# Kernel tuning notes

Hardware: AMD Instinct MI355X
Metric: run time of the kernel (lower is better)

## Reference

```python
import jax, jax.numpy as jnp
import numpy as np

MAX_NODES = 1024
FEAT = 64
HID = 32
B, S = 32, 4096


def setup_inputs() -> dict:
    key = jax.random.key(0)
    ks = jax.random.split(key, 9)
    flow_features = jax.random.normal(ks[0], (B, S, FEAT), dtype=jnp.float32)
    src_ips = jax.random.randint(ks[1], (B, S), 0, MAX_NODES, dtype=jnp.int32)
    dst_ips = jax.random.randint(ks[2], (B, S), 0, MAX_NODES, dtype=jnp.int32)
    flow_volumes = jax.random.uniform(ks[3], (B, S), dtype=jnp.float32)
    # learned parameters
    node_emb = jax.random.normal(ks[4], (MAX_NODES, FEAT), dtype=jnp.float32)
    W1 = jax.random.normal(ks[5], (2 * FEAT, HID), dtype=jnp.float32) * (1.0 / np.sqrt(2 * FEAT))
    b1 = jnp.zeros((HID,), dtype=jnp.float32)
    W2 = jax.random.normal(ks[6], (HID, 1), dtype=jnp.float32) * (1.0 / np.sqrt(HID))
    b2 = jnp.zeros((1,), dtype=jnp.float32)
    return {"flow_features": flow_features, "src_ips": src_ips, "dst_ips": dst_ips,
            "flow_volumes": flow_volumes, "node_emb": node_emb,
            "W1": W1, "b1": b1, "W2": W2, "b2": b2}


def reference(flow_features, src_ips, dst_ips, flow_volumes, node_emb, W1, b1, W2, b2):
    b_, s_, f_ = flow_features.shape
    n_ = node_emb.shape[0]
    bidx = jnp.arange(b_)[:, None]  # (B,1) broadcast over seq

    # ---- scatter-add flow features into destination nodes ----
    node_features = jnp.zeros((b_, n_, f_), dtype=flow_features.dtype)
    node_features = node_features.at[bidx, dst_ips].add(flow_features)
    # F.normalize(p=2, dim=-1): x / max(||x||, eps)
    norm = jnp.linalg.norm(node_features, axis=-1, keepdims=True)
    node_features = node_features / jnp.maximum(norm, 1e-12)

    # ---- gather embeddings, edge MLP, scatter weights into adjacency ----
    src_e = node_emb[src_ips]  # (B,S,F)
    dst_e = node_emb[dst_ips]  # (B,S,F)
    h = jax.nn.relu(jnp.concatenate([src_e, dst_e], axis=-1) @ W1 + b1)  # (B,S,32)
    edge_w = jax.nn.sigmoid((h @ W2 + b2)[..., 0])  # (B,S)
    vol_w = jax.nn.sigmoid(flow_volumes / 1000.0)
    w = edge_w * vol_w  # (B,S)

    adjacency = jnp.zeros((b_, n_, n_), dtype=flow_features.dtype)
    # semantics up to scatter ordering of colliding edges)
    adjacency = adjacency.at[bidx, src_ips, dst_ips].set(w)
    adjacency = adjacency.at[bidx, dst_ips, src_ips].set(w)
    return node_features, adjacency
```

## Files before the change

### kernel.cpp

```cpp
#include <hip/hip_runtime.h>
#include <cstdint>
#include <cstddef>

#define BB 32
#define SS 4096
#define FEAT_ 64
#define HID_ 32
#define NN 1024
#define RPB 8

typedef int v4i __attribute__((ext_vector_type(4)));

__global__ void node_feat_kernel(const float* __restrict__ flow,
                                 const int* __restrict__ dst,
                                 float* __restrict__ nf) {
    int row0 = blockIdx.x << 4;
    int b = row0 >> 10;
    __shared__ int sdst[SS];

    const int4* g = (const int4*)(dst + (size_t)b * SS);
    int4* sd4 = (int4*)sdst;
    for (int i = threadIdx.x; i < SS / 4; i += 256) sd4[i] = g[i];
    __syncthreads();

    int wave = threadIdx.x >> 6;
    int lane = threadIdx.x & 63;
    int r0 = row0 + (wave << 2);
    int node0 = r0 & (NN - 1);
    const float* fb = flow + ((size_t)b * SS << 6);

    float acc[4] = {0.f, 0.f, 0.f, 0.f};
    for (int s0 = 0; s0 < SS; s0 += 64) {
        int d = sdst[s0 + lane];
        #pragma unroll
        for (int j = 0; j < 4; ++j) {
            unsigned long long m = __ballot(d == node0 + j);
            while (m) {
                int bit = __ffsll((long long)m) - 1;
                m &= m - 1;
                acc[j] += fb[((s0 + bit) << 6) + lane];
            }
        }
    }

    #pragma unroll
    for (int j = 0; j < 4; ++j) {
        float ss = acc[j] * acc[j];
        #pragma unroll
        for (int off = 32; off > 0; off >>= 1) ss += __shfl_xor(ss, off, 64);
        float v = acc[j] / fmaxf(sqrtf(ss), 1e-12f);
        __builtin_nontemporal_store(v, &nf[((size_t)(r0 + j) << 6) + lane]);
    }
}

__global__ void mlp_kernel(const int* __restrict__ src,
                           const int* __restrict__ dst,
                           const float* __restrict__ vol,
                           const float* __restrict__ emb,
                           const float* __restrict__ W1,
                           const float* __restrict__ b1,
                           const float* __restrict__ W2,
                           const float* __restrict__ b2,
                           float* __restrict__ wout) {
    int i = blockIdx.x * blockDim.x + threadIdx.x;
    int si = src[i], di = dst[i];

    float acc[HID_];
    #pragma unroll
    for (int j = 0; j < HID_; ++j) acc[j] = b1[j];

    #pragma unroll
    for (int half = 0; half < 2; ++half) {
        const float* e = emb + ((half ? di : si) << 6);
        const float* w = W1 + half * 64 * HID_;
        for (int k = 0; k < 64; k += 4) {
            float4 v = *(const float4*)(e + k);
            #pragma unroll
            for (int j = 0; j < HID_; ++j) {
                float a = acc[j];
                a += v.x * w[(k + 0) * HID_ + j];
                a += v.y * w[(k + 1) * HID_ + j];
                a += v.z * w[(k + 2) * HID_ + j];
                a += v.w * w[(k + 3) * HID_ + j];
                acc[j] = a;
            }
        }
    }

    float dotv = b2[0];
    #pragma unroll
    for (int j = 0; j < HID_; ++j) dotv += fmaxf(acc[j], 0.0f) * W2[j];
    float edge_w = 1.0f / (1.0f + expf(-dotv));
    float vol_w  = 1.0f / (1.0f + expf(-vol[i] / 1000.0f));
    wout[i] = edge_w * vol_w;
}

__global__ void adj_dense_kernel(const int* __restrict__ src,
                                 const int* __restrict__ dst,
                                 const float* __restrict__ wbuf,
                                 float* __restrict__ adj) {
    int b  = blockIdx.x >> 7;
    int r0 = (blockIdx.x & 127) << 3;
    int tid = threadIdx.x;

    __shared__ int D[RPB * NN];

    const int* sb = src + (size_t)b * SS;
    const int* db = dst + (size_t)b * SS;
    int svr[16], dvr[16];
    #pragma unroll
    for (int i = 0; i < 16; ++i) {
        svr[i] = sb[tid + (i << 8)];
        dvr[i] = db[tid + (i << 8)];
    }

    int4* D4 = (int4*)D;
    int4 z; z.x = z.y = z.z = z.w = 0;
    #pragma unroll
    for (int i = 0; i < RPB * NN / 4 / 256; ++i) D4[tid + i * 256] = z;
    __syncthreads();

    #pragma unroll
    for (int i = 0; i < 16; ++i) {
        int s = tid + (i << 8);
        unsigned lr1 = (unsigned)(svr[i] - r0);
        if (lr1 < RPB) atomicMax(&D[(lr1 << 10) + dvr[i]], s + 1);
        unsigned lr2 = (unsigned)(dvr[i] - r0);
        if (lr2 < RPB) atomicMax(&D[(lr2 << 10) + svr[i]], SS + s + 1);
    }
    __syncthreads();

    const float* wb = wbuf + (size_t)b * SS;
    #pragma unroll
    for (int i = 0; i < 16; ++i) {
        int s = tid + (i << 8);
        unsigned lr1 = (unsigned)(svr[i] - r0);
        unsigned lr2 = (unsigned)(dvr[i] - r0);
        if ((lr1 < RPB) | (lr2 < RPB)) {
            int wbits = __float_as_int(wb[s]);
            if (lr1 < RPB && D[(lr1 << 10) + dvr[i]] == s + 1)
                D[(lr1 << 10) + dvr[i]] = wbits;
            if (lr2 < RPB && D[(lr2 << 10) + svr[i]] == SS + s + 1)
                D[(lr2 << 10) + svr[i]] = wbits;
        }
    }
    __syncthreads();

    const v4i* Df = (const v4i*)D;
    v4i* out = (v4i*)(adj + ((size_t)b * NN + r0) * NN);
    #pragma unroll
    for (int i = 0; i < RPB * NN / 4 / 256; ++i)
        __builtin_nontemporal_store(Df[tid + i * 256], &out[tid + i * 256]);
}

extern "C" void kernel_launch(void* const* d_in, const int* in_sizes, int n_in,
                              void* d_out, int out_size, void* d_ws, size_t ws_size,
                              hipStream_t stream) {
    const float* flow = (const float*)d_in[0];
    const int*   src  = (const int*)d_in[1];
    const int*   dst  = (const int*)d_in[2];
    const float* vol  = (const float*)d_in[3];
    const float* emb  = (const float*)d_in[4];
    const float* W1   = (const float*)d_in[5];
    const float* b1   = (const float*)d_in[6];
    const float* W2   = (const float*)d_in[7];
    const float* b2   = (const float*)d_in[8];

    float* nf  = (float*)d_out;
    float* adj = nf + (size_t)BB * NN * FEAT_;
    float* wbuf = (float*)d_ws;

    mlp_kernel<<<(BB * SS) / 256, 256, 0, stream>>>(src, dst, vol, emb,
                                                    W1, b1, W2, b2, wbuf);
    adj_dense_kernel<<<BB * (NN / RPB), 256, 0, stream>>>(src, dst, wbuf, adj);
    node_feat_kernel<<<(BB * NN) / 16, 256, 0, stream>>>(flow, dst, nf);
}
```

Before: 240.5 us.

## Precompute per-node W1 projections and fuse edge MLP with node-feature kernel

Result: faster. 225.5 us (-6.2%).

```diff
diff --git a/kernel.cpp b/kernel.cpp
--- a/kernel.cpp
+++ b/kernel.cpp
@@ -9,31 +9,80 @@
 #define NN 1024
 #define RPB 8
 
+#define EDGE_BLOCKS ((BB * SS) / 256)
+#define NF_BLOCKS   ((BB * NN) / 32)
+
 typedef int v4i __attribute__((ext_vector_type(4)));
 
-__global__ void node_feat_kernel(const float* __restrict__ flow,
-                                 const int* __restrict__ dst,
-                                 float* __restrict__ nf) {
-    int row0 = blockIdx.x << 4;
+__global__ void ab_kernel(const float* __restrict__ emb,
+                          const float* __restrict__ W1,
+                          const float* __restrict__ b1,
+                          float* __restrict__ ab) {
+    int idx = blockIdx.x * 256 + threadIdx.x;
+    int n = idx >> 6;
+    int c = idx & 63;
+    int half = c >> 5, j = c & 31;
+    const float* e = emb + (n << 6);
+    const float* w = W1 + (half << 11) + j;
+    float acc = half ? 0.0f : b1[j];
+    #pragma unroll
+    for (int k = 0; k < 64; ++k)
+        acc = fmaf(e[k], w[k << 5], acc);
+    ab[idx] = acc;
+}
+
+__global__ void nf_edge_kernel(const float* __restrict__ flow,
+                               const int* __restrict__ src,
+                               const int* __restrict__ dst,
+                               const float* __restrict__ vol,
+                               const float* __restrict__ ab,
+                               const float* __restrict__ W2,
+                               const float* __restrict__ b2,
+                               float* __restrict__ nf,
+                               float* __restrict__ wout) {
+    if (blockIdx.x < EDGE_BLOCKS) {
+        int i = blockIdx.x * 256 + threadIdx.x;
+        int si = src[i], di = dst[i];
+        const float4* As = (const float4*)(ab + (si << 6));
+        const float4* Bd = (const float4*)(ab + (di << 6) + HID_);
+        float dotv = b2[0];
+        #pragma unroll
+        for (int q = 0; q < 8; ++q) {
+            float4 a  = As[q];
+            float4 bv = Bd[q];
+            float4 wv = *(const float4*)(W2 + (q << 2));
+            dotv += fmaxf(a.x + bv.x, 0.0f) * wv.x;
+            dotv += fmaxf(a.y + bv.y, 0.0f) * wv.y;
+            dotv += fmaxf(a.z + bv.z, 0.0f) * wv.z;
+            dotv += fmaxf(a.w + bv.w, 0.0f) * wv.w;
+        }
+        float edge_w = 1.0f / (1.0f + expf(-dotv));
+        float vol_w  = 1.0f / (1.0f + expf(-vol[i] / 1000.0f));
+        wout[i] = edge_w * vol_w;
+        return;
+    }
+
+    int nb = blockIdx.x - EDGE_BLOCKS;
+    int row0 = nb << 5;
     int b = row0 >> 10;
     __shared__ int sdst[SS];
 
     const int4* g = (const int4*)(dst + (size_t)b * SS);
     int4* sd4 = (int4*)sdst;
-    for (int i = threadIdx.x; i < SS / 4; i += 256) sd4[i] = g[i];
+    for (int t = threadIdx.x; t < SS / 4; t += 256) sd4[t] = g[t];
     __syncthreads();
 
     int wave = threadIdx.x >> 6;
     int lane = threadIdx.x & 63;
-    int r0 = row0 + (wave << 2);
+    int r0 = row0 + (wave << 3);
     int node0 = r0 & (NN - 1);
     const float* fb = flow + ((size_t)b * SS << 6);
 
-    float acc[4] = {0.f, 0.f, 0.f, 0.f};
+    float acc[8] = {0.f, 0.f, 0.f, 0.f, 0.f, 0.f, 0.f, 0.f};
     for (int s0 = 0; s0 < SS; s0 += 64) {
         int d = sdst[s0 + lane];
         #pragma unroll
-        for (int j = 0; j < 4; ++j) {
+        for (int j = 0; j < 8; ++j) {
             unsigned long long m = __ballot(d == node0 + j);
             while (m) {
                 int bit = __ffsll((long long)m) - 1;
@@ -44,55 +93,13 @@
     }
 
     #pragma unroll
-    for (int j = 0; j < 4; ++j) {
+    for (int j = 0; j < 8; ++j) {
         float ss = acc[j] * acc[j];
         #pragma unroll
         for (int off = 32; off > 0; off >>= 1) ss += __shfl_xor(ss, off, 64);
         float v = acc[j] / fmaxf(sqrtf(ss), 1e-12f);
         __builtin_nontemporal_store(v, &nf[((size_t)(r0 + j) << 6) + lane]);
     }
-}
-
-__global__ void mlp_kernel(const int* __restrict__ src,
-                           const int* __restrict__ dst,
-                           const float* __restrict__ vol,
-                           const float* __restrict__ emb,
-                           const float* __restrict__ W1,
-                           const float* __restrict__ b1,
-                           const float* __restrict__ W2,
-                           const float* __restrict__ b2,
-                           float* __restrict__ wout) {
-    int i = blockIdx.x * blockDim.x + threadIdx.x;
-    int si = src[i], di = dst[i];
-
-    float acc[HID_];
-    #pragma unroll
-    for (int j = 0; j < HID_; ++j) acc[j] = b1[j];
-
-    #pragma unroll
-    for (int half = 0; half < 2; ++half) {
-        const float* e = emb + ((half ? di : si) << 6);
-        const float* w = W1 + half * 64 * HID_;
-        for (int k = 0; k < 64; k += 4) {
-            float4 v = *(const float4*)(e + k);
-            #pragma unroll
-            for (int j = 0; j < HID_; ++j) {
-                float a = acc[j];
-                a += v.x * w[(k + 0) * HID_ + j];
-                a += v.y * w[(k + 1) * HID_ + j];
-                a += v.z * w[(k + 2) * HID_ + j];
-                a += v.w * w[(k + 3) * HID_ + j];
-                acc[j] = a;
-            }
-        }
-    }
-
-    float dotv = b2[0];
-    #pragma unroll
-    for (int j = 0; j < HID_; ++j) dotv += fmaxf(acc[j], 0.0f) * W2[j];
-    float edge_w = 1.0f / (1.0f + expf(-dotv));
-    float vol_w  = 1.0f / (1.0f + expf(-vol[i] / 1000.0f));
-    wout[i] = edge_w * vol_w;
 }
 
 __global__ void adj_dense_kernel(const int* __restrict__ src,
@@ -166,12 +173,18 @@
     const float* W2   = (const float*)d_in[7];
     const float* b2   = (const float*)d_in[8];
 
-    float* nf  = (float*)d_out;
-    float* adj = nf + (size_t)BB * NN * FEAT_;
+    float* nf   = (float*)d_out;
+    float* adj  = nf + (size_t)BB * NN * FEAT_;
     float* wbuf = (float*)d_ws;
 
-    mlp_kernel<<<(BB * SS) / 256, 256, 0, stream>>>(src, dst, vol, emb,
-                                                    W1, b1, W2, b2, wbuf);
+    float* ab;
+    if (ws_size >= (size_t)(BB * SS + NN * 64) * sizeof(float))
+        ab = wbuf + (size_t)BB * SS;
+    else
+        ab = adj + (size_t)BB * NN * NN - (size_t)NN * 64;
+
+    ab_kernel<<<(NN * 64) / 256, 256, 0, stream>>>(emb, W1, b1, ab);
+    nf_edge_kernel<<<EDGE_BLOCKS + NF_BLOCKS, 256, 0, stream>>>(
+        flow, src, dst, vol, ab, W2, b2, nf, wbuf);
     adj_dense_kernel<<<BB * (NN / RPB), 256, 0, stream>>>(src, dst, wbuf, adj);
-    node_feat_kernel<<<(BB * NN) / 16, 256, 0, stream>>>(flow, dst, nf);
 }
```
